# Performance work log

Measured on AMD Instinct MI355X. Metric: run time of the kernel, lower is better.

The kernel has to match this reference:

```python
import jax, jax.numpy as jnp
import numpy as np

B, T, IN, H, OUT = 64, 32, 256, 512, 256
M, W, R = 256, 64, 4            # nr_cells, cell_size, read_heads
NN_IN = IN + R * W              # 512
NN_OUT = H + R * W              # 768
IFACE = R * W + 3 * W + 5 * R + 3  # 471
CLIP = 20.0
DELTA = 1e-6


def setup_inputs():
    key = jax.random.key(0)
    ks = jax.random.split(key, 10)
    s = 0.05
    bound = float(np.sqrt(6.0 / (B * H + 2 * H)))  # xavier_uniform on (2,B,H)
    return {
        'x': jax.random.normal(ks[0], (B, T, IN), jnp.float32),
        'h0': jax.random.uniform(ks[1], (2, B, H), jnp.float32, -bound, bound),
        'Wih0': jax.random.normal(ks[2], (4 * H, NN_IN), jnp.float32) * s,
        'Whh0': jax.random.normal(ks[3], (4 * H, H), jnp.float32) * s,
        'bih0': jnp.zeros((4 * H,), jnp.float32),
        'bhh0': jnp.zeros((4 * H,), jnp.float32),
        'Wih1': jax.random.normal(ks[4], (4 * H, H), jnp.float32) * s,
        'Whh1': jax.random.normal(ks[5], (4 * H, H), jnp.float32) * s,
        'bih1': jnp.zeros((4 * H,), jnp.float32),
        'bhh1': jnp.zeros((4 * H,), jnp.float32),
        'Wif': jax.random.normal(ks[6], (IFACE, H), jnp.float32) * s,
        'bif': jnp.zeros((IFACE,), jnp.float32),
        'Wout': jax.random.normal(ks[7], (OUT, NN_OUT), jnp.float32) * s,
        'bout': jnp.zeros((OUT,), jnp.float32),
    }


def _lstm_cell(x, h, c, Wih, Whh, bih, bhh):
    g = x @ Wih.T + bih + h @ Whh.T + bhh
    i, f, gg, o = jnp.split(g, 4, axis=1)  # torch gate order i,f,g,o
    c = jax.nn.sigmoid(f) * c + jax.nn.sigmoid(i) * jnp.tanh(gg)
    h = jax.nn.sigmoid(o) * jnp.tanh(c)
    return h, c


def _content_weights(mem, keys, strengths):
    # mem: (b,M,W), keys: (b,K,W), strengths: (b,K) -> softmax over M
    mem_n = mem / (jnp.linalg.norm(mem, axis=2, keepdims=True) + DELTA)
    key_n = keys / (jnp.linalg.norm(keys, axis=2, keepdims=True) + DELTA)
    sim = jnp.einsum('bkw,bmw->bkm', key_n, mem_n)
    return jax.nn.softmax(sim * strengths[..., None], axis=2)


def _memory_step(xi, mem, link, prec, rw, ww, usage):
    b = xi.shape[0]
    o = 0
    rk = jnp.tanh(xi[:, :R * W].reshape(b, R, W)); o = R * W
    rs = jax.nn.softplus(xi[:, o:o + R]); o += R
    wk = jnp.tanh(xi[:, o:o + W]).reshape(b, 1, W); o += W
    ws = jax.nn.softplus(xi[:, o])[:, None]; o += 1
    ev = jax.nn.sigmoid(xi[:, o:o + W]); o += W
    wv = jnp.tanh(xi[:, o:o + W]); o += W
    fg = jax.nn.sigmoid(xi[:, o:o + R]); o += R
    ag = jax.nn.sigmoid(xi[:, o])[:, None]; o += 1
    wg = jax.nn.sigmoid(xi[:, o])[:, None]; o += 1
    rm = jax.nn.softmax(xi[:, o:o + 3 * R].reshape(b, R, 3), axis=2)

    # usage update (uses OLD read/write weights); single write head
    usage = usage + (1.0 - usage) * ww
    psi = jnp.prod(1.0 - fg[:, :, None] * rw, axis=1)
    usage = usage * psi

    # write content addressing on OLD memory
    wcw = _content_weights(mem, wk, ws)[:, 0]  # (b,M)

    # allocation by ascending sort of usage (exclusive cumprod)
    u = DELTA + (1.0 - DELTA) * usage
    phi = jnp.argsort(u, axis=1)
    sorted_u = jnp.take_along_axis(u, phi, axis=1)
    excl = jnp.cumprod(jnp.concatenate([jnp.ones((b, 1), u.dtype), sorted_u], axis=1), axis=1)[:, :-1]
    sorted_alloc = (1.0 - sorted_u) * excl
    alloc = jnp.take_along_axis(sorted_alloc, jnp.argsort(phi, axis=1), axis=1)

    ww = wg * (ag * alloc + (1.0 - ag) * wcw)  # (b,M)

    # erase + write
    mem = mem * (1.0 - ww[:, :, None] * ev[:, None, :]) + ww[:, :, None] * wv[:, None, :]

    # temporal link matrix + precedence
    prev_scale = 1.0 - ww[:, :, None] - ww[:, None, :]
    link = prev_scale * link + ww[:, :, None] * prec[:, None, :]
    link = link * (1.0 - jnp.eye(M, dtype=link.dtype))
    prec = (1.0 - ww.sum(axis=1, keepdims=True)) * prec + ww

    # read: directional weights use NEW link and OLD read weights; content uses NEW memory
    rcw = _content_weights(mem, rk, rs)               # (b,R,M)
    fwd = jnp.einsum('bij,brj->bri', link, rw)
    bwd = jnp.einsum('brj,bji->bri', rw, link)
    rw = rm[:, :, 0:1] * bwd + rm[:, :, 1:2] * fwd + rm[:, :, 2:3] * rcw
    rvec = jnp.einsum('brm,bmw->brw', rw, mem).reshape(b, R * W)
    return rvec, mem, link, prec, rw, ww, usage


def reference(x, h0, Wih0, Whh0, bih0, bhh0, Wih1, Whh1, bih1, bhh1, Wif, bif, Wout, bout):
    b = x.shape[0]
    lr0 = jnp.zeros((b, R * W), x.dtype)  # initial last_read; NOTE: source concatenates this
    # initial zero last_read to EVERY timestep's controller input (inputs built upfront)
    carry0 = (h0[0], h0[0], h0[1], h0[1],
              jnp.full((b, M, W), DELTA, x.dtype),   # memory
              jnp.zeros((b, M, M), x.dtype),          # link matrix
              jnp.zeros((b, M), x.dtype),             # precedence
              jnp.full((b, R, M), DELTA, x.dtype),    # read weights
              jnp.full((b, M), DELTA, x.dtype),       # write weights
              jnp.zeros((b, M), x.dtype))             # usage

    def step(carry, x_t):
        h0_, c0_, h1_, c1_, mem, link, prec, rw, ww, usage = carry
        inp = jnp.concatenate([x_t, lr0], axis=1)
        h0_, c0_ = _lstm_cell(inp, h0_, c0_, Wih0, Whh0, bih0, bhh0)
        h1_, c1_ = _lstm_cell(h0_, h1_, c1_, Wih1, Whh1, bih1, bhh1)
        out = jnp.clip(h1_, -CLIP, CLIP)
        xi = out @ Wif.T + bif
        rvec, mem, link, prec, rw, ww, usage = _memory_step(xi, mem, link, prec, rw, ww, usage)
        o_t = jnp.concatenate([out, rvec], axis=1)  # (b, NN_OUT)
        return (h0_, c0_, h1_, c1_, mem, link, prec, rw, ww, usage), o_t

    _, ys = jax.lax.scan(step, carry0, jnp.swapaxes(x, 0, 1))  # (T,b,NN_OUT)
    outputs = jnp.tanh(ys) @ Wout.T + bout  # Dropout(p=0) -> Tanh -> Linear
    return jnp.swapaxes(outputs, 0, 1)      # (b,T,OUT)
```

## Files before the change

### kernel.cpp

```cpp
#include <hip/hip_runtime.h>
#include <hip/hip_bf16.h>
#include <math.h>


typedef __bf16 bf16_t;
typedef __attribute__((ext_vector_type(8))) __bf16 bf16x8;
typedef __attribute__((ext_vector_type(4))) float f32x4;

#define B_    64
#define T_    32
#define IN_   256
#define H_    512
#define M_    256
#define W_    64
#define R_    4
#define IFACE_ 471
#define DELTA_ 1e-6f

#define OFF_H0SEQ  (0L)
#define SZ_H0SEQ   (32L*64*512*2)
#define OFF_OUTSEQ (OFF_H0SEQ + SZ_H0SEQ)
#define SZ_OUTSEQ  (32L*64*512*2)
#define OFF_H0BUF  (OFF_OUTSEQ + SZ_OUTSEQ)
#define SZ_HBUF    (2L*64*512*2)
// ... 135 lines not shown
  v0=__expf(v0-mx); v1=__expf(v1-mx); v2=__expf(v2-mx); v3=__expf(v3-mx);
  float s = v0+v1+v2+v3;
  #pragma unroll
  for (int off=32; off; off>>=1) s += __shfl_xor(s, off, 64);
  float inv = frcp(s);
  a[lane]=v0*inv; a[64+lane]=v1*inv; a[128+lane]=v2*inv; a[192+lane]=v3*inv;
}

struct ProdShm {
  bf16_t wpool[66560];
  float  cst[64][16];
  float  bias[4][16];
};
struct ConsShm {
  float smem[256][65];
  float xib[480];
  float rkn4r[2][65][4];
  float wkn[64], ev_[64], wvv[64];
  float rs_[4], fg_[4], rm_[4][3];
  float wsS, agS, wgS, wwsumS;
  float invn[256], wcw[256];
  float usage[256], uu[256], su[256], scanA[256];
  int   rank_[256];
  float ww_[256], prec_[256];
  float rw_[4][256];
  float rw4[256][4];
  float fwd_[4][256], bwd_[4][256], rcw_[4][256];
  bf16_t rwb[4][264];
  bf16_t wwb[256], precb[256];
  float p2cT[2][264];
  float p5cT[5][2][264];
  float rvp[8][4][64];
};
union ShUnion { ProdShm p; ConsShm c; };

__global__ __launch_bounds__(512) void k_main(
    const bf16_t* __restrict__ xb, const bf16_t* __restrict__ h0b,
    const bf16_t* __restrict__ W0, const bf16_t* __restrict__ W1,
    const bf16_t* __restrict__ W2, const bf16_t* __restrict__ W3,
    const float* __restrict__ bs0, const float* __restrict__ bs1,
    const bf16_t* __restrict__ Wifp, const float* __restrict__ bifp,
    bf16_t* __restrict__ h0buf, bf16_t* __restrict__ h1buf,
    bf16_t* __restrict__ h0seq, bf16_t* __restrict__ outseq,
    float* __restrict__ XI, float* __restrict__ RVEC,
    unsigned* __restrict__ flg)
{
  __shared__ ShUnion sh;
  const int bid = blockIdx.x;
  const int tid = threadIdx.x, lane = tid & 63, wv = tid >> 6;
  const int m16 = lane & 15, q = lane >> 4;

  if (bid < 64){
    ProdShm& P = sh.p;
    const int layer = bid >> 5;
    const int u0 = (bid & 31) * 16;

    if (!layer){
      for (int i = tid; i < 64*32; i += 512){
        int rl = i >> 5, c8 = (i & 31)*8;
        int grow = (rl >> 4)*512 + u0 + (rl & 15);
        *(bf16x8*)&P.wpool[rl*264 + c8] = *(const bf16x8*)(W0 + (size_t)grow*512 + c8);
      }
      for (int i = tid; i < 64*64; i += 512){
        int rl = i >> 6, c8 = (i & 63)*8;
        int grow = (rl >> 4)*512 + u0 + (rl & 15);
        *(bf16x8*)&P.wpool[16896 + rl*520 + c8] = *(const bf16x8*)(W1 + (size_t)grow*512 + c8);
      }
    } else {
      for (int i = tid; i < 64*64; i += 512){
        int rl = i >> 6, c8 = (i & 63)*8;
        int grow = (rl >> 4)*512 + u0 + (rl & 15);
        *(bf16x8*)&P.wpool[rl*520 + c8]         = *(const bf16x8*)(W2 + (size_t)grow*512 + c8);
        *(bf16x8*)&P.wpool[33280 + rl*520 + c8] = *(const bf16x8*)(W3 + (size_t)grow*512 + c8);
      }
    }
    for (int i = tid; i < 64*16; i += 512){
      int b = i >> 4, n = i & 15;
      P.cst[b][n] = (float)h0b[layer*(64*512) + b*512 + u0 + n];
    }
    if (tid < 64){
      int G = tid >> 4, n = tid & 15;
      const float* bs = layer ? bs1 : bs0;
      P.bias[G][n] = bs[G*512 + u0 + n];
    }
    __syncthreads();

    bf16_t* hbuf = layer ? h1buf : h0buf;

    for (int ps = 0; ps <= 33; ++ps){
      if (wv < 4){
        const int t = layer ? (ps - 1) : ps;
        const bool active = layer ? (ps >= 1 && ps <= 32) : (ps < 32);
        if (active){
          const int p = t & 1;
          const bf16_t* hin = hbuf + p*(64*512);
          bf16_t* hout = hbuf + (p^1)*(64*512);
          const int b0 = wv * 16;

          f32x4 acc[4];
          #pragma unroll
          for (int G = 0; G < 4; ++G){ float bv = P.bias[G][m16]; acc[G] = (f32x4){bv,bv,bv,bv}; }

          if (!layer){
            #pragma unroll 2
            for (int kt = 0; kt < 8; ++kt){
              bf16x8 a = *(const bf16x8*)(xb + ((size_t)(b0+m16)*T_ + t)*IN_ + kt*32 + q*8);
              #pragma unroll
              for (int G = 0; G < 4; ++G)
                acc[G] = __builtin_amdgcn_mfma_f32_16x16x32_bf16(
                    a, *(const bf16x8*)&P.wpool[(G*16+m16)*264 + kt*32 + q*8], acc[G], 0, 0, 0);
            }
            #pragma unroll 4
            for (int kt = 0; kt < 16; ++kt){
              bf16x8 a = *(const bf16x8*)(hin + (b0+m16)*512 + kt*32 + q*8);
              #pragma unroll
              for (int G = 0; G < 4; ++G)
                acc[G] = __builtin_amdgcn_mfma_f32_16x16x32_bf16(
                    a, *(const bf16x8*)&P.wpool[16896 + (G*16+m16)*520 + kt*32 + q*8], acc[G], 0, 0, 0);
            }
          } else {
            #pragma unroll 4
            for (int kt = 0; kt < 16; ++kt){
              bf16x8 a = *(const bf16x8*)(h0seq + ((size_t)t*64 + b0+m16)*512 + kt*32 + q*8);
              #pragma unroll
              for (int G = 0; G < 4; ++G)
                acc[G] = __builtin_amdgcn_mfma_f32_16x16x32_bf16(
                    a, *(const bf16x8*)&P.wpool[(G*16+m16)*520 + kt*32 + q*8], acc[G], 0, 0, 0);
            }
            #pragma unroll 4
            for (int kt = 0; kt < 16; ++kt){
              bf16x8 a = *(const bf16x8*)(hin + (b0+m16)*512 + kt*32 + q*8);
              #pragma unroll
              for (int G = 0; G < 4; ++G)
                acc[G] = __builtin_amdgcn_mfma_f32_16x16x32_bf16(
                    a, *(const bf16x8*)&P.wpool[33280 + (G*16+m16)*520 + kt*32 + q*8], acc[G], 0, 0, 0);
            }
          }
          #pragma unroll
          for (int v = 0; v < 4; ++v){
            int b = b0 + q*4 + v;
            float gi = acc[0][v], gf = acc[1][v], gg = acc[2][v], go = acc[3][v];
            float c_ = sigf(gf)*P.cst[b][m16] + sigf(gi)*tanh_f(gg);
            P.cst[b][m16] = c_;
            float h = sigf(go)*tanh_f(c_);
            bf16_t hb = (bf16_t)h;
            hout[b*512 + u0 + m16] = hb;
            if (!layer) h0seq[((size_t)t*64 + b)*512 + u0 + m16] = hb;
            else        outseq[((size_t)t*64 + b)*512 + u0 + m16] = hb;
          }
        }
      } else if (ps >= 2 && bid < 30){
        const int t2 = ps - 2;
        const int b0 = (wv - 4) * 16;
        const int r = bid*16 + m16;
        float bv = bifp[r];
        f32x4 acc = {bv,bv,bv,bv};
        const bf16_t* arow = outseq + ((size_t)t2*64 + b0 + m16)*512 + q*8;
        const bf16_t* brow = Wifp + (size_t)r*512 + q*8;
        #pragma unroll 4
        for (int kt = 0; kt < 16; ++kt){
          acc = __builtin_amdgcn_mfma_f32_16x16x32_bf16(
              *(const bf16x8*)(arow + kt*32), *(const bf16x8*)(brow + kt*32), acc, 0, 0, 0);
        }
        #pragma unroll
        for (int v = 0; v < 4; ++v)
          XI[((size_t)t2*64 + b0 + q*4 + v)*480 + r] = acc[v];
      }
      flagbar(flg, bid, (unsigned)(ps + 1), tid, lane, wv);
    }
  } else {
    ConsShm& S = sh.c;
    const int b = bid - 64;
    const int quad = lane >> 4, li = lane & 15;

    bf16x8 rowL[2][8], colL[2][8];
    #pragma unroll
    for (int g = 0; g < 2; ++g)
      #pragma unroll
      for (int ch = 0; ch < 8; ++ch)
        #pragma unroll
        for (int z = 0; z < 8; ++z){ rowL[g][ch][z] = (bf16_t)0.0f; colL[g][ch][z] = (bf16_t)0.0f; }

    float mr[32];
    #pragma unroll
    for (int z = 0; z < 32; ++z) mr[z] = DELTA_;

    if (tid < 256){
      S.ww_[tid] = DELTA_; S.usage[tid] = 0.0f; S.prec_[tid] = 0.0f;
      S.invn[tid] = 1.0f/(fsqrt_(64.0f*DELTA_*DELTA_) + DELTA_);
      S.wwb[tid] = (bf16_t)DELTA_; S.precb[tid] = (bf16_t)0.0f;
      #pragma unroll
      for (int r = 0; r < 4; ++r) S.rw_[r][tid] = DELTA_;
    }
    for (int i = tid; i < 4*264; i += 512) ((bf16_t*)S.rwb)[i] = (bf16_t)DELTA_;
    for (int i = tid; i < 256*65; i += 512) ((float*)S.smem)[i] = DELTA_;
    __syncthreads();

    const int mH = tid >> 1, q2 = tid & 1;

    for (int t = 0; t < 32; ++t){
      { const unsigned tgt = (unsigned)(t + 3);
        if (wv == 0){
          for (;;){
            unsigned f = flag_ld(flg + (size_t)lane*16);
            if (__all(f >= tgt)) break;
            __builtin_amdgcn_s_sleep(2);
          }
          __builtin_amdgcn_fence(__ATOMIC_ACQUIRE, "agent");
        }
        __syncthreads();
      }
      if (tid < IFACE_) S.xib[tid] = XI[((size_t)t*64 + b)*480 + tid];
      __syncthreads();

      if (wv < 4){
        float v = tanh_f(S.xib[wv*64 + lane]);
        float s = wred(v*v);
        float vn = v * frcp(fsqrt_(s) + DELTA_);
        S.rkn4r[0][lane][wv] = vn; S.rkn4r[1][lane][wv] = vn;
      } else if (wv == 4){
        float v = tanh_f(S.xib[260 + lane]);
        float s = wred(v*v);
        S.wkn[lane] = v * frcp(fsqrt_(s) + DELTA_);
      } else if (wv == 5){ S.ev_[lane] = sigf(S.xib[325 + lane]);
      } else if (wv == 6){ S.wvv[lane] = tanh_f(S.xib[389 + lane]);
      } else {
        if (lane < 4)        S.rs_[lane] = softplusf(S.xib[256 + lane]);
        else if (lane == 4)  S.wsS = softplusf(S.xib[324]);
        else if (lane < 9)   S.fg_[lane-5] = sigf(S.xib[453 + (lane-5)]);
        else if (lane == 9)  S.agS = sigf(S.xib[457]);
        else if (lane == 10) S.wgS = sigf(S.xib[458]);
        else if (lane >= 16 && lane < 20){
          int r = lane - 16;
          float a0 = S.xib[459+r*3], a1 = S.xib[459+r*3+1], a2 = S.xib[459+r*3+2];
          float mx = fmaxf(a0, fmaxf(a1, a2));
          float e0 = __expf(a0-mx), e1 = __expf(a1-mx), e2 = __expf(a2-mx);
          float inv = frcp(e0+e1+e2);
          S.rm_[r][0]=e0*inv; S.rm_[r][1]=e1*inv; S.rm_[r][2]=e2*inv;
        }
      }
      __syncthreads();

      if (tid < 256){
        int m = tid;
        float us = S.usage[m] + (1.0f - S.usage[m])*S.ww_[m];
        float psi = (1.0f - S.fg_[0]*S.rw_[0][m]) * (1.0f - S.fg_[1]*S.rw_[1][m])
                  * (1.0f - S.fg_[2]*S.rw_[2][m]) * (1.0f - S.fg_[3]*S.rw_[3][m]);
        us *= psi;
        S.usage[m] = us;
        S.uu[m] = DELTA_ + (1.0f - DELTA_)*us;
      }
      { float acc = 0.0f;
        #pragma unroll
        for (int it = 0; it < 32; ++it){
          int w = q2*32 + it;
          acc += mr[it] * S.wkn[w];
        }
        S.p2cT[q2][mH] = acc; }
      __syncthreads();

      if (wv == 0){
        #pragma unroll
        for (int z = 0; z < 4; ++z){
          int m = z*64 + lane;
          S.wcw[m] = S.wsS * (S.p2cT[0][m] + S.p2cT[1][m]) * S.invn[m];
        }
        softmax256_wave(S.wcw, lane);
      } else if (tid >= 256){
        const int i = tid - 256;
        const float ui = S.uu[i];
        int cnt = 0;
        #pragma unroll 8
        for (int k = 0; k < 64; ++k){
          f32x4 u4 = *(const f32x4*)&S.uu[k*4];
          #pragma unroll
          for (int z = 0; z < 4; ++z){
            int j = k*4 + z; float uj = u4[z];
            cnt += (uj < ui || (uj == ui && j < i)) ? 1 : 0;
          }
        }
        S.rank_[i] = cnt;
        S.su[cnt] = ui;
      }
      __syncthreads();

      if (wv == 0){
        int base = lane*4;
        float v0 = S.su[base], v1 = S.su[base+1], v2 = S.su[base+2];
        float p1 = v0*v1, p2 = p1*v2, p3 = p2*S.su[base+3];
        float sc = p3;
        #pragma unroll
        for (int off = 1; off < 64; off <<= 1){
          float n = __shfl_up(sc, off, 64);
          if (lane >= off) sc *= n;
        }
        float exch = __shfl_up(sc, 1, 64);
        if (lane == 0) exch = 1.0f;
        S.scanA[base] = exch; S.scanA[base+1] = exch*v0;
        S.scanA[base+2] = exch*p1; S.scanA[base+3] = exch*p2;
      }
      __syncthreads();

      { const int m = mH;
        float al = (1.0f - S.uu[m]) * S.scanA[S.rank_[m]];
        float wm = S.wgS*(S.agS*al + (1.0f - S.agS)*S.wcw[m]);
        if (q2 == 0){ S.ww_[m] = wm; S.wwb[m] = (bf16_t)wm; }
        float s2 = 0.0f, sr0 = 0.0f, sr1 = 0.0f, sr2 = 0.0f, sr3 = 0.0f;
        #pragma unroll
        for (int it = 0; it < 32; ++it){
          int w = q2*32 + it;
          float mn = mr[it]*(1.0f - wm*S.ev_[w]) + wm*S.wvv[w];
          mr[it] = mn;
          S.smem[m][w] = mn;
          s2 += mn*mn;
          f32x4 rk = *(const f32x4*)&S.rkn4r[q2][w][0];
          sr0 += mn*rk[0]; sr1 += mn*rk[1]; sr2 += mn*rk[2]; sr3 += mn*rk[3];
        }
        S.p5cT[0][q2][m] = s2;
        S.p5cT[1][q2][m] = sr0; S.p5cT[2][q2][m] = sr1;
        S.p5cT[3][q2][m] = sr2; S.p5cT[4][q2][m] = sr3; }
      __syncthreads();

      if (tid < 256){
        int m = tid;
        float s2 = S.p5cT[0][0][m] + S.p5cT[0][1][m];
        float inv = frcp(fsqrt_(s2) + DELTA_);
        S.invn[m] = inv;
        #pragma unroll
        for (int r = 0; r < 4; ++r){
          float sr = S.p5cT[r+1][0][m] + S.p5cT[r+1][1][m];
          S.rcw_[r][m] = S.rs_[r]*sr*inv;
        }
      } else if (wv == 4){
        float s = wred(S.ww_[lane] + S.ww_[64+lane] + S.ww_[128+lane] + S.ww_[192+lane]);
        if (lane == 0) S.wwsumS = s;
      }
      __syncthreads();

      { float wown[2], pown[2], alpha[2];
        #pragma unroll
        for (int g = 0; g < 2; ++g){
          int o = wv*32 + g*16 + li;
          wown[g] = (float)S.wwb[o]; pown[g] = (float)S.precb[o];
          alpha[g] = 1.0f - wown[g];
        }
        f32x4 facc[2] = {{0,0,0,0},{0,0,0,0}}, bacc[2] = {{0,0,0,0},{0,0,0,0}};
        #pragma unroll
        for (int ch = 0; ch < 8; ++ch){
          const int cbase = ch*32 + quad*8;
          bf16x8 rwf = *(const bf16x8*)&S.rwb[li & 3][cbase];
          bf16x8 wwv = *(const bf16x8*)&S.wwb[cbase];
          bf16x8 pcv = *(const bf16x8*)&S.precb[cbase];
          float wcf[8], pcf[8];
          #pragma unroll
          for (int jj = 0; jj < 8; ++jj){ wcf[jj] = (float)wwv[jj]; pcf[jj] = (float)pcv[jj]; }
          #pragma unroll
          for (int g = 0; g < 2; ++g){
            const int o = wv*32 + g*16 + li;
            bf16x8 rl = rowL[g][ch];
            bf16x8 cl = colL[g][ch];
            #pragma unroll
            for (int jj = 0; jj < 8; ++jj){
              const int c = cbase + jj;
              float s = alpha[g] - wcf[jj];
              float vr = s*(float)rl[jj] + wown[g]*pcf[jj];
              float vc = s*(float)cl[jj] + wcf[jj]*pown[g];
              if (c == o){ vr = 0.0f; vc = 0.0f; }
              rl[jj] = (bf16_t)vr;
              cl[jj] = (bf16_t)vc;
            }
            rowL[g][ch] = rl; colL[g][ch] = cl;
            facc[g] = __builtin_amdgcn_mfma_f32_16x16x32_bf16(rl, rwf, facc[g], 0, 0, 0);
            bacc[g] = __builtin_amdgcn_mfma_f32_16x16x32_bf16(rwf, cl, bacc[g], 0, 0, 0);
          }
        }
        #pragma unroll
        for (int g = 0; g < 2; ++g){
          if (li < 4){
            #pragma unroll
            for (int z = 0; z < 4; ++z) S.fwd_[li][wv*32 + g*16 + quad*4 + z] = facc[g][z];
          }
          if (quad == 0){
            #pragma unroll
            for (int z = 0; z < 4; ++z) S.bwd_[z][wv*32 + g*16 + li] = bacc[g][z];
          }
        }
      }
      __syncthreads();

      if (wv < 4) softmax256_wave(S.rcw_[wv], lane);
      else {
        int m = tid - 256;
        float p = (1.0f - S.wwsumS)*S.prec_[m] + S.ww_[m];
        S.prec_[m] = p;
        S.precb[m] = (bf16_t)p;
      }
      __syncthreads();

      { int r = tid >> 7, m0 = (tid & 127)*2;
        #pragma unroll
        for (int z = 0; z < 2; ++z){
          int m = m0 + z;
          float v = S.rm_[r][0]*S.bwd_[r][m] + S.rm_[r][1]*S.fwd_[r][m] + S.rm_[r][2]*S.rcw_[r][m];
          S.rw_[r][m] = v;
          S.rw4[m][r] = v;
          S.rwb[r][m] = (bf16_t)v;
        } }
      __syncthreads();

      { float r0 = 0, r1 = 0, r2 = 0, r3 = 0;
        #pragma unroll
        for (int k = 0; k < 32; ++k){
          int m = wv*32 + k;
          f32x4 r4 = *(const f32x4*)&S.rw4[m][0];
          float mv = S.smem[m][lane];
          r0 += r4[0]*mv; r1 += r4[1]*mv; r2 += r4[2]*mv; r3 += r4[3]*mv;
        }
        S.rvp[wv][0][lane] = r0; S.rvp[wv][1][lane] = r1;
        S.rvp[wv][2][lane] = r2; S.rvp[wv][3][lane] = r3; }
      __syncthreads();

      if (tid < 256){
        const int w = tid & 63, r = tid >> 6;
        float v = 0.0f;
        #pragma unroll
        for (int c = 0; c < 8; ++c) v += S.rvp[c][r][w];
        RVEC[((size_t)t*64 + b)*256 + tid] = v;
      }
      __syncthreads();
    }
  }
}

__global__ void k_tanhy(const bf16_t* __restrict__ outseq, const float* __restrict__ RVEC,
                        bf16_t* __restrict__ Y){
  const int n = 2048*768;
  for (int i = blockIdx.x*blockDim.x + threadIdx.x; i < n; i += gridDim.x*blockDim.x){
    int row = i / 768, j = i - row*768;
    float v = (j < 512) ? (float)outseq[(size_t)row*512 + j] : RVEC[(size_t)row*256 + (j - 512)];
    Y[i] = (bf16_t)tanh_f(v);
  }
}

__global__ __launch_bounds__(256,1) void k_out(
    const bf16_t* __restrict__ Y, const bf16_t* __restrict__ Woutb,
    const float* __restrict__ boutf, void* __restrict__ dout,
    const int* __restrict__ flag)
{
  const int mf = *flag;
  const int mt = blockIdx.x;
  const int tid = threadIdx.x, lane = tid & 63, wv = tid >> 6;
  const int nt = blockIdx.y*4 + wv;
  const int m16 = lane & 15, q = lane >> 4;
  const int o = nt*16 + m16;
  float bv = boutf[o];
  f32x4 acc = {bv,bv,bv,bv};
  const bf16_t* arow = Y + (size_t)(mt*16 + m16)*768 + q*8;
  const bf16_t* brow = Woutb + (size_t)o*768 + q*8;
  for (int kt = 0; kt < 24; ++kt){
    acc = __builtin_amdgcn_mfma_f32_16x16x32_bf16(
        *(const bf16x8*)(arow + kt*32), *(const bf16x8*)(brow + kt*32), acc, 0, 0, 0);
  }
  #pragma unroll
// ... 10 lines not shown
                              void* d_out, int out_size, void* d_ws, size_t ws_size,
                              hipStream_t stream)
{
  char* ws = (char*)d_ws;
  bf16_t* H0SEQ  = (bf16_t*)(ws + OFF_H0SEQ);
  bf16_t* OUTSEQ = (bf16_t*)(ws + OFF_OUTSEQ);
  bf16_t* H0BUF  = (bf16_t*)(ws + OFF_H0BUF);
  bf16_t* H1BUF  = (bf16_t*)(ws + OFF_H1BUF);
  float*  XI     = (float*) (ws + OFF_XI);
  float*  RVEC   = (float*) (ws + OFF_RVEC);
  bf16_t* YBF    = (bf16_t*)(ws + OFF_YBF);
  unsigned* BAR  = (unsigned*)(ws + OFF_BAR);
  int*    FLAG   = (int*)   (ws + OFF_BAR + 8);
  bf16_t* XB     = (bf16_t*)(ws + OFF_XB);
  bf16_t* H0B    = (bf16_t*)(ws + OFF_H0B);
  bf16_t* W0     = (bf16_t*)(ws + OFF_W0);
  bf16_t* W1     = (bf16_t*)(ws + OFF_W1);
  bf16_t* W2     = (bf16_t*)(ws + OFF_W2);
  bf16_t* W3     = (bf16_t*)(ws + OFF_W3);
  bf16_t* WIFP   = (bf16_t*)(ws + OFF_WIF);
  bf16_t* WOUTB  = (bf16_t*)(ws + OFF_WOUTB);
  float*  BS0    = (float*) (ws + OFF_BS0);
  float*  BS1    = (float*) (ws + OFF_BS1);
  float*  BIFP   = (float*) (ws + OFF_BIF);
  float*  BOUTF  = (float*) (ws + OFF_BOUTF);
  unsigned* FLG  = (unsigned*)(ws + OFF_FLG);

  k_detect<<<1, 256, 0, stream>>>((const unsigned short*)d_in[0], FLAG, BAR, FLG);
  k_convert<<<dim3(256, 9), 256, 0, stream>>>(
      d_in[0], d_in[1], d_in[2], d_in[3], d_in[4], d_in[5], d_in[6],
      d_in[7], d_in[8], d_in[9], d_in[10], d_in[11], d_in[12], d_in[13],
      XB, H0B, H0BUF, H1BUF, W0, W1, W2, W3, WIFP, WOUTB,
      BS0, BS1, BIFP, BOUTF, FLAG);
  k_main<<<128, 512, 0, stream>>>(XB, H0B, W0, W1, W2, W3, BS0, BS1,
                                  WIFP, BIFP, H0BUF, H1BUF, H0SEQ, OUTSEQ,
                                  XI, RVEC, FLG);
  k_tanhy<<<512, 256, 0, stream>>>(OUTSEQ, RVEC, YBF);
  k_out<<<dim3(128, 4), 256, 0, stream>>>(YBF, WOUTB, BOUTF, d_out, FLAG);
}
```

Measured before the change: 1.057 ms.

## Split fused persistent LSTM/memory kernel into separate LSTM, interface and memory kernels

Replaces the single persistent kernel, where 64 producer blocks ran the two LSTM layers and 64 consumer blocks ran the DNC memory update behind flag-based polling, with three sequential launches. The LSTM kernel keeps the grid-wide flag barrier but drops the interface-projection waves. The interface GEMM becomes its own fully parallel grid over timesteps. The memory kernel runs all 32 steps without waiting on flags. This removes cross-block polling and the idle half-warps in producer blocks, but gives up the overlap between the LSTM recurrence and the memory recurrence, so the two serial chains now run back to back.

```diff
diff --git a/kernel.cpp b/kernel.cpp
--- a/kernel.cpp
+++ b/kernel.cpp
@@ -191,403 +191,396 @@
   float p5cT[5][2][264];
   float rvp[8][4][64];
 };
-union ShUnion { ProdShm p; ConsShm c; };
-
-__global__ __launch_bounds__(512) void k_main(
+
+__global__ __launch_bounds__(256) void k_lstm(
     const bf16_t* __restrict__ xb, const bf16_t* __restrict__ h0b,
     const bf16_t* __restrict__ W0, const bf16_t* __restrict__ W1,
     const bf16_t* __restrict__ W2, const bf16_t* __restrict__ W3,
     const float* __restrict__ bs0, const float* __restrict__ bs1,
-    const bf16_t* __restrict__ Wifp, const float* __restrict__ bifp,
     bf16_t* __restrict__ h0buf, bf16_t* __restrict__ h1buf,
     bf16_t* __restrict__ h0seq, bf16_t* __restrict__ outseq,
-    float* __restrict__ XI, float* __restrict__ RVEC,
     unsigned* __restrict__ flg)
 {
-  __shared__ ShUnion sh;
+  __shared__ ProdShm P;
   const int bid = blockIdx.x;
   const int tid = threadIdx.x, lane = tid & 63, wv = tid >> 6;
   const int m16 = lane & 15, q = lane >> 4;
-
-  if (bid < 64){
-    ProdShm& P = sh.p;
-    const int layer = bid >> 5;
-    const int u0 = (bid & 31) * 16;
-
-    if (!layer){
-      for (int i = tid; i < 64*32; i += 512){
-        int rl = i >> 5, c8 = (i & 31)*8;
-        int grow = (rl >> 4)*512 + u0 + (rl & 15);
-        *(bf16x8*)&P.wpool[rl*264 + c8] = *(const bf16x8*)(W0 + (size_t)grow*512 + c8);
-      }
-      for (int i = tid; i < 64*64; i += 512){
-        int rl = i >> 6, c8 = (i & 63)*8;
-        int grow = (rl >> 4)*512 + u0 + (rl & 15);
-        *(bf16x8*)&P.wpool[16896 + rl*520 + c8] = *(const bf16x8*)(W1 + (size_t)grow*512 + c8);
-      }
-    } else {
-      for (int i = tid; i < 64*64; i += 512){
-        int rl = i >> 6, c8 = (i & 63)*8;
-        int grow = (rl >> 4)*512 + u0 + (rl & 15);
-        *(bf16x8*)&P.wpool[rl*520 + c8]         = *(const bf16x8*)(W2 + (size_t)grow*512 + c8);
-        *(bf16x8*)&P.wpool[33280 + rl*520 + c8] = *(const bf16x8*)(W3 + (size_t)grow*512 + c8);
-      }
-    }
-    for (int i = tid; i < 64*16; i += 512){
-      int b = i >> 4, n = i & 15;
-      P.cst[b][n] = (float)h0b[layer*(64*512) + b*512 + u0 + n];
-    }
-    if (tid < 64){
-      int G = tid >> 4, n = tid & 15;
-      const float* bs = layer ? bs1 : bs0;
-      P.bias[G][n] = bs[G*512 + u0 + n];
-    }
-    __syncthreads();
-
-    bf16_t* hbuf = layer ? h1buf : h0buf;
-
-    for (int ps = 0; ps <= 33; ++ps){
-      if (wv < 4){
-        const int t = layer ? (ps - 1) : ps;
-        const bool active = layer ? (ps >= 1 && ps <= 32) : (ps < 32);
-        if (active){
-          const int p = t & 1;
-          const bf16_t* hin = hbuf + p*(64*512);
-          bf16_t* hout = hbuf + (p^1)*(64*512);
-          const int b0 = wv * 16;
-
-          f32x4 acc[4];
+  const int layer = bid >> 5;
+  const int u0 = (bid & 31) * 16;
+
+  if (!layer){
+    for (int i = tid; i < 64*32; i += 256){
+      int rl = i >> 5, c8 = (i & 31)*8;
+      int grow = (rl >> 4)*512 + u0 + (rl & 15);
+      *(bf16x8*)&P.wpool[rl*264 + c8] = *(const bf16x8*)(W0 + (size_t)grow*512 + c8);
+    }
+    for (int i = tid; i < 64*64; i += 256){
+      int rl = i >> 6, c8 = (i & 63)*8;
+      int grow = (rl >> 4)*512 + u0 + (rl & 15);
+      *(bf16x8*)&P.wpool[16896 + rl*520 + c8] = *(const bf16x8*)(W1 + (size_t)grow*512 + c8);
+    }
+  } else {
+    for (int i = tid; i < 64*64; i += 256){
+      int rl = i >> 6, c8 = (i & 63)*8;
+      int grow = (rl >> 4)*512 + u0 + (rl & 15);
+      *(bf16x8*)&P.wpool[rl*520 + c8]         = *(const bf16x8*)(W2 + (size_t)grow*512 + c8);
+      *(bf16x8*)&P.wpool[33280 + rl*520 + c8] = *(const bf16x8*)(W3 + (size_t)grow*512 + c8);
+    }
+  }
+  for (int i = tid; i < 64*16; i += 256){
+    int b = i >> 4, n = i & 15;
+    P.cst[b][n] = (float)h0b[layer*(64*512) + b*512 + u0 + n];
+  }
+  if (tid < 64){
+    int G = tid >> 4, n = tid & 15;
+    const float* bs = layer ? bs1 : bs0;
+    P.bias[G][n] = bs[G*512 + u0 + n];
+  }
+  __syncthreads();
+
+  bf16_t* hbuf = layer ? h1buf : h0buf;
+
+  for (int ps = 0; ps <= 32; ++ps){
+    const int t = layer ? (ps - 1) : ps;
+    const bool active = layer ? (ps >= 1) : (ps < 32);
+    if (active){
+      const int p = t & 1;
+      const bf16_t* hin = hbuf + p*(64*512);
+      bf16_t* hout = hbuf + (p^1)*(64*512);
+      const int b0 = wv * 16;
+
+      f32x4 acc[4];
+      #pragma unroll
+      for (int G = 0; G < 4; ++G){ float bv = P.bias[G][m16]; acc[G] = (f32x4){bv,bv,bv,bv}; }
+
+      if (!layer){
+        #pragma unroll 2
+        for (int kt = 0; kt < 8; ++kt){
+          bf16x8 a = *(const bf16x8*)(xb + ((size_t)(b0+m16)*T_ + t)*IN_ + kt*32 + q*8);
           #pragma unroll
-          for (int G = 0; G < 4; ++G){ float bv = P.bias[G][m16]; acc[G] = (f32x4){bv,bv,bv,bv}; }
-
-          if (!layer){
-            #pragma unroll 2
-            for (int kt = 0; kt < 8; ++kt){
-              bf16x8 a = *(const bf16x8*)(xb + ((size_t)(b0+m16)*T_ + t)*IN_ + kt*32 + q*8);
-              #pragma unroll
-              for (int G = 0; G < 4; ++G)
-                acc[G] = __builtin_amdgcn_mfma_f32_16x16x32_bf16(
-                    a, *(const bf16x8*)&P.wpool[(G*16+m16)*264 + kt*32 + q*8], acc[G], 0, 0, 0);
-            }
-            #pragma unroll 4
-            for (int kt = 0; kt < 16; ++kt){
-              bf16x8 a = *(const bf16x8*)(hin + (b0+m16)*512 + kt*32 + q*8);
-              #pragma unroll
-              for (int G = 0; G < 4; ++G)
-                acc[G] = __builtin_amdgcn_mfma_f32_16x16x32_bf16(
-                    a, *(const bf16x8*)&P.wpool[16896 + (G*16+m16)*520 + kt*32 + q*8], acc[G], 0, 0, 0);
-            }
-          } else {
-            #pragma unroll 4
-            for (int kt = 0; kt < 16; ++kt){
-              bf16x8 a = *(const bf16x8*)(h0seq + ((size_t)t*64 + b0+m16)*512 + kt*32 + q*8);
-              #pragma unroll
-              for (int G = 0; G < 4; ++G)
-                acc[G] = __builtin_amdgcn_mfma_f32_16x16x32_bf16(
-                    a, *(const bf16x8*)&P.wpool[(G*16+m16)*520 + kt*32 + q*8], acc[G], 0, 0, 0);
-            }
-            #pragma unroll 4
-            for (int kt = 0; kt < 16; ++kt){
-              bf16x8 a = *(const bf16x8*)(hin + (b0+m16)*512 + kt*32 + q*8);
-              #pragma unroll
-              for (int G = 0; G < 4; ++G)
-                acc[G] = __builtin_amdgcn_mfma_f32_16x16x32_bf16(
-                    a, *(const bf16x8*)&P.wpool[33280 + (G*16+m16)*520 + kt*32 + q*8], acc[G], 0, 0, 0);
-            }
-          }
-          #pragma unroll
-          for (int v = 0; v < 4; ++v){
-            int b = b0 + q*4 + v;
-            float gi = acc[0][v], gf = acc[1][v], gg = acc[2][v], go = acc[3][v];
-            float c_ = sigf(gf)*P.cst[b][m16] + sigf(gi)*tanh_f(gg);
-            P.cst[b][m16] = c_;
-            float h = sigf(go)*tanh_f(c_);
-            bf16_t hb = (bf16_t)h;
-            hout[b*512 + u0 + m16] = hb;
-            if (!layer) h0seq[((size_t)t*64 + b)*512 + u0 + m16] = hb;
-            else        outseq[((size_t)t*64 + b)*512 + u0 + m16] = hb;
-          }
-        }
-      } else if (ps >= 2 && bid < 30){
-        const int t2 = ps - 2;
-        const int b0 = (wv - 4) * 16;
-        const int r = bid*16 + m16;
-        float bv = bifp[r];
-        f32x4 acc = {bv,bv,bv,bv};
-        const bf16_t* arow = outseq + ((size_t)t2*64 + b0 + m16)*512 + q*8;
-        const bf16_t* brow = Wifp + (size_t)r*512 + q*8;
+          for (int G = 0; G < 4; ++G)
+            acc[G] = __builtin_amdgcn_mfma_f32_16x16x32_bf16(
+                a, *(const bf16x8*)&P.wpool[(G*16+m16)*264 + kt*32 + q*8], acc[G], 0, 0, 0);
+        }
         #pragma unroll 4
         for (int kt = 0; kt < 16; ++kt){
-          acc = __builtin_amdgcn_mfma_f32_16x16x32_bf16(
-              *(const bf16x8*)(arow + kt*32), *(const bf16x8*)(brow + kt*32), acc, 0, 0, 0);
-        }
-        #pragma unroll
-        for (int v = 0; v < 4; ++v)
-          XI[((size_t)t2*64 + b0 + q*4 + v)*480 + r] = acc[v];
-      }
-      flagbar(flg, bid, (unsigned)(ps + 1), tid, lane, wv);
-    }
-  } else {
-    ConsShm& S = sh.c;
-    const int b = bid - 64;
-    const int quad = lane >> 4, li = lane & 15;
-
-    bf16x8 rowL[2][8], colL[2][8];
+          bf16x8 a = *(const bf16x8*)(hin + (b0+m16)*512 + kt*32 + q*8);
+          #pragma unroll
+          for (int G = 0; G < 4; ++G)
+            acc[G] = __builtin_amdgcn_mfma_f32_16x16x32_bf16(
+                a, *(const bf16x8*)&P.wpool[16896 + (G*16+m16)*520 + kt*32 + q*8], acc[G], 0, 0, 0);
+        }
+      } else {
+        #pragma unroll 4
+        for (int kt = 0; kt < 16; ++kt){
+          bf16x8 a = *(const bf16x8*)(h0seq + ((size_t)t*64 + b0+m16)*512 + kt*32 + q*8);
+          #pragma unroll
+          for (int G = 0; G < 4; ++G)
+            acc[G] = __builtin_amdgcn_mfma_f32_16x16x32_bf16(
+                a, *(const bf16x8*)&P.wpool[(G*16+m16)*520 + kt*32 + q*8], acc[G], 0, 0, 0);
+        }
+        #pragma unroll 4
+        for (int kt = 0; kt < 16; ++kt){
+          bf16x8 a = *(const bf16x8*)(hin + (b0+m16)*512 + kt*32 + q*8);
+          #pragma unroll
+          for (int G = 0; G < 4; ++G)
+            acc[G] = __builtin_amdgcn_mfma_f32_16x16x32_bf16(
+                a, *(const bf16x8*)&P.wpool[33280 + (G*16+m16)*520 + kt*32 + q*8], acc[G], 0, 0, 0);
+        }
+      }
+      #pragma unroll
+      for (int v = 0; v < 4; ++v){
+        int b = b0 + q*4 + v;
+        float gi = acc[0][v], gf = acc[1][v], gg = acc[2][v], go = acc[3][v];
+        float c_ = sigf(gf)*P.cst[b][m16] + sigf(gi)*tanh_f(gg);
+        P.cst[b][m16] = c_;
+        float h = sigf(go)*tanh_f(c_);
+        bf16_t hb = (bf16_t)h;
+        hout[b*512 + u0 + m16] = hb;
+        if (!layer) h0seq[((size_t)t*64 + b)*512 + u0 + m16] = hb;
+        else        outseq[((size_t)t*64 + b)*512 + u0 + m16] = hb;
+      }
+    }
+    if (ps < 32) flagbar(flg, bid, (unsigned)(ps + 1), tid, lane, wv);
+  }
+}
+
+__global__ __launch_bounds__(256) void k_xi(
+    const bf16_t* __restrict__ outseq, const bf16_t* __restrict__ Wifp,
+    const float* __restrict__ bifp, float* __restrict__ XI)
+{
+  const int rt = blockIdx.x;
+  const int t2 = blockIdx.y;
+  const int tid = threadIdx.x, lane = tid & 63, wv = tid >> 6;
+  const int m16 = lane & 15, q = lane >> 4;
+  const int b0 = wv * 16;
+  const int r = rt*16 + m16;
+  float bv = bifp[r];
+  f32x4 acc = {bv,bv,bv,bv};
+  const bf16_t* arow = outseq + ((size_t)t2*64 + b0 + m16)*512 + q*8;
+  const bf16_t* brow = Wifp + (size_t)r*512 + q*8;
+  #pragma unroll 4
+  for (int kt = 0; kt < 16; ++kt){
+    acc = __builtin_amdgcn_mfma_f32_16x16x32_bf16(
+        *(const bf16x8*)(arow + kt*32), *(const bf16x8*)(brow + kt*32), acc, 0, 0, 0);
+  }
+  #pragma unroll
+  for (int v = 0; v < 4; ++v)
+    XI[((size_t)t2*64 + b0 + q*4 + v)*480 + r] = acc[v];
+}
+
+__global__ __launch_bounds__(512) void k_mem(
+    const float* __restrict__ XI, float* __restrict__ RVEC)
+{
+  __shared__ ConsShm S;
+  const int b = blockIdx.x;
+  const int tid = threadIdx.x, lane = tid & 63, wv = tid >> 6;
+  const int quad = lane >> 4, li = lane & 15;
+
+  bf16x8 rowL[2][8], colL[2][8];
+  #pragma unroll
+  for (int g = 0; g < 2; ++g)
     #pragma unroll
-    for (int g = 0; g < 2; ++g)
-      #pragma unroll
-      for (int ch = 0; ch < 8; ++ch)
-        #pragma unroll
-        for (int z = 0; z < 8; ++z){ rowL[g][ch][z] = (bf16_t)0.0f; colL[g][ch][z] = (bf16_t)0.0f; }
-
-    float mr[32];
+    for (int ch = 0; ch < 8; ++ch)
+      #pragma unroll
+      for (int z = 0; z < 8; ++z){ rowL[g][ch][z] = (bf16_t)0.0f; colL[g][ch][z] = (bf16_t)0.0f; }
+
+  float mr[32];
+  #pragma unroll
+  for (int z = 0; z < 32; ++z) mr[z] = DELTA_;
+
+  if (tid < 256){
+    S.ww_[tid] = DELTA_; S.usage[tid] = 0.0f; S.prec_[tid] = 0.0f;
+    S.invn[tid] = 1.0f/(fsqrt_(64.0f*DELTA_*DELTA_) + DELTA_);
+    S.wwb[tid] = (bf16_t)DELTA_; S.precb[tid] = (bf16_t)0.0f;
     #pragma unroll
-    for (int z = 0; z < 32; ++z) mr[z] = DELTA_;
+    for (int r = 0; r < 4; ++r) S.rw_[r][tid] = DELTA_;
+  }
+  for (int i = tid; i < 4*264; i += 512) ((bf16_t*)S.rwb)[i] = (bf16_t)DELTA_;
+  for (int i = tid; i < 256*65; i += 512) ((float*)S.smem)[i] = DELTA_;
+  __syncthreads();
+
+  const int mH = tid >> 1, q2 = tid & 1;
+
+  for (int t = 0; t < 32; ++t){
+    if (tid < IFACE_) S.xib[tid] = XI[((size_t)t*64 + b)*480 + tid];
+    __syncthreads();
+
+    if (wv < 4){
+      float v = tanh_f(S.xib[wv*64 + lane]);
+      float s = wred(v*v);
+      float vn = v * frcp(fsqrt_(s) + DELTA_);
+      S.rkn4r[0][lane][wv] = vn; S.rkn4r[1][lane][wv] = vn;
+    } else if (wv == 4){
+      float v = tanh_f(S.xib[260 + lane]);
+      float s = wred(v*v);
+      S.wkn[lane] = v * frcp(fsqrt_(s) + DELTA_);
+    } else if (wv == 5){ S.ev_[lane] = sigf(S.xib[325 + lane]);
+    } else if (wv == 6){ S.wvv[lane] = tanh_f(S.xib[389 + lane]);
+    } else {
+      if (lane < 4)        S.rs_[lane] = softplusf(S.xib[256 + lane]);
+      else if (lane == 4)  S.wsS = softplusf(S.xib[324]);
+      else if (lane < 9)   S.fg_[lane-5] = sigf(S.xib[453 + (lane-5)]);
+      else if (lane == 9)  S.agS = sigf(S.xib[457]);
+      else if (lane == 10) S.wgS = sigf(S.xib[458]);
+      else if (lane >= 16 && lane < 20){
+        int r = lane - 16;
+        float a0 = S.xib[459+r*3], a1 = S.xib[459+r*3+1], a2 = S.xib[459+r*3+2];
+        float mx = fmaxf(a0, fmaxf(a1, a2));
+        float e0 = __expf(a0-mx), e1 = __expf(a1-mx), e2 = __expf(a2-mx);
+        float inv = frcp(e0+e1+e2);
+        S.rm_[r][0]=e0*inv; S.rm_[r][1]=e1*inv; S.rm_[r][2]=e2*inv;
+      }
+    }
+    __syncthreads();
 
     if (tid < 256){
-      S.ww_[tid] = DELTA_; S.usage[tid] = 0.0f; S.prec_[tid] = 0.0f;
-      S.invn[tid] = 1.0f/(fsqrt_(64.0f*DELTA_*DELTA_) + DELTA_);
-      S.wwb[tid] = (bf16_t)DELTA_; S.precb[tid] = (bf16_t)0.0f;
-      #pragma unroll
-      for (int r = 0; r < 4; ++r) S.rw_[r][tid] = DELTA_;
-    }
-    for (int i = tid; i < 4*264; i += 512) ((bf16_t*)S.rwb)[i] = (bf16_t)DELTA_;
-    for (int i = tid; i < 256*65; i += 512) ((float*)S.smem)[i] = DELTA_;
-    __syncthreads();
-
-    const int mH = tid >> 1, q2 = tid & 1;
-
-    for (int t = 0; t < 32; ++t){
-      { const unsigned tgt = (unsigned)(t + 3);
-        if (wv == 0){
-          for (;;){
-            unsigned f = flag_ld(flg + (size_t)lane*16);
-            if (__all(f >= tgt)) break;
-            __builtin_amdgcn_s_sleep(2);
-          }
-          __builtin_amdgcn_fence(__ATOMIC_ACQUIRE, "agent");
-        }
-        __syncthreads();
-      }
-      if (tid < IFACE_) S.xib[tid] = XI[((size_t)t*64 + b)*480 + tid];
-      __syncthreads();
-
-      if (wv < 4){
-        float v = tanh_f(S.xib[wv*64 + lane]);
-        float s = wred(v*v);
-        float vn = v * frcp(fsqrt_(s) + DELTA_);
-        S.rkn4r[0][lane][wv] = vn; S.rkn4r[1][lane][wv] = vn;
-      } else if (wv == 4){
-        float v = tanh_f(S.xib[260 + lane]);
-        float s = wred(v*v);
-        S.wkn[lane] = v * frcp(fsqrt_(s) + DELTA_);
-      } else if (wv == 5){ S.ev_[lane] = sigf(S.xib[325 + lane]);
-      } else if (wv == 6){ S.wvv[lane] = tanh_f(S.xib[389 + lane]);
-      } else {
-        if (lane < 4)        S.rs_[lane] = softplusf(S.xib[256 + lane]);
-        else if (lane == 4)  S.wsS = softplusf(S.xib[324]);
-        else if (lane < 9)   S.fg_[lane-5] = sigf(S.xib[453 + (lane-5)]);
-        else if (lane == 9)  S.agS = sigf(S.xib[457]);
-        else if (lane == 10) S.wgS = sigf(S.xib[458]);
-        else if (lane >= 16 && lane < 20){
-          int r = lane - 16;
-          float a0 = S.xib[459+r*3], a1 = S.xib[459+r*3+1], a2 = S.xib[459+r*3+2];
-          float mx = fmaxf(a0, fmaxf(a1, a2));
-          float e0 = __expf(a0-mx), e1 = __expf(a1-mx), e2 = __expf(a2-mx);
-          float inv = frcp(e0+e1+e2);
-          S.rm_[r][0]=e0*inv; S.rm_[r][1]=e1*inv; S.rm_[r][2]=e2*inv;
-        }
-      }
-      __syncthreads();
-
-      if (tid < 256){
-        int m = tid;
-        float us = S.usage[m] + (1.0f - S.usage[m])*S.ww_[m];
-        float psi = (1.0f - S.fg_[0]*S.rw_[0][m]) * (1.0f - S.fg_[1]*S.rw_[1][m])
-                  * (1.0f - S.fg_[2]*S.rw_[2][m]) * (1.0f - S.fg_[3]*S.rw_[3][m]);
-        us *= psi;
-        S.usage[m] = us;
-        S.uu[m] = DELTA_ + (1.0f - DELTA_)*us;
-      }
-      { float acc = 0.0f;
-        #pragma unroll
-        for (int it = 0; it < 32; ++it){
-          int w = q2*32 + it;
-          acc += mr[it] * S.wkn[w];
-        }
-        S.p2cT[q2][mH] = acc; }
-      __syncthreads();
-
-      if (wv == 0){
+      int m = tid;
+      float us = S.usage[m] + (1.0f - S.usage[m])*S.ww_[m];
+      float psi = (1.0f - S.fg_[0]*S.rw_[0][m]) * (1.0f - S.fg_[1]*S.rw_[1][m])
+                * (1.0f - S.fg_[2]*S.rw_[2][m]) * (1.0f - S.fg_[3]*S.rw_[3][m]);
+      us *= psi;
+      S.usage[m] = us;
+      S.uu[m] = DELTA_ + (1.0f - DELTA_)*us;
+    }
+    { float acc = 0.0f;
+      #pragma unroll
+      for (int it = 0; it < 32; ++it){
+        int w = q2*32 + it;
+        acc += mr[it] * S.wkn[w];
+      }
+      S.p2cT[q2][mH] = acc; }
+    __syncthreads();
+
+    if (wv == 0){
+      #pragma unroll
+      for (int z = 0; z < 4; ++z){
+        int m = z*64 + lane;
+        S.wcw[m] = S.wsS * (S.p2cT[0][m] + S.p2cT[1][m]) * S.invn[m];
+      }
+      softmax256_wave(S.wcw, lane);
+    } else if (tid >= 256){
+      const int i = tid - 256;
+      const float ui = S.uu[i];
+      int cnt = 0;
+      #pragma unroll 8
+      for (int k = 0; k < 64; ++k){
+        f32x4 u4 = *(const f32x4*)&S.uu[k*4];
         #pragma unroll
         for (int z = 0; z < 4; ++z){
-          int m = z*64 + lane;
-          S.wcw[m] = S.wsS * (S.p2cT[0][m] + S.p2cT[1][m]) * S.invn[m];
-        }
-        softmax256_wave(S.wcw, lane);
-      } else if (tid >= 256){
-        const int i = tid - 256;
-        const float ui = S.uu[i];
-        int cnt = 0;
-        #pragma unroll 8
-        for (int k = 0; k < 64; ++k){
-          f32x4 u4 = *(const f32x4*)&S.uu[k*4];
-          #pragma unroll
-          for (int z = 0; z < 4; ++z){
-            int j = k*4 + z; float uj = u4[z];
-            cnt += (uj < ui || (uj == ui && j < i)) ? 1 : 0;
-          }
-        }
-        S.rank_[i] = cnt;
-        S.su[cnt] = ui;
-      }
-      __syncthreads();
-
-      if (wv == 0){
-        int base = lane*4;
-        float v0 = S.su[base], v1 = S.su[base+1], v2 = S.su[base+2];
-        float p1 = v0*v1, p2 = p1*v2, p3 = p2*S.su[base+3];
-        float sc = p3;
+          int j = k*4 + z; float uj = u4[z];
+          cnt += (uj < ui || (uj == ui && j < i)) ? 1 : 0;
+        }
+      }
+      S.rank_[i] = cnt;
+      S.su[cnt] = ui;
+    }
+    __syncthreads();
+
+    if (wv == 0){
+      int base = lane*4;
+      float v0 = S.su[base], v1 = S.su[base+1], v2 = S.su[base+2];
+      float p1 = v0*v1, p2 = p1*v2, p3 = p2*S.su[base+3];
+      float sc = p3;
+      #pragma unroll
+      for (int off = 1; off < 64; off <<= 1){
+        float n = __shfl_up(sc, off, 64);
+        if (lane >= off) sc *= n;
+      }
+      float exch = __shfl_up(sc, 1, 64);
+      if (lane == 0) exch = 1.0f;
+      S.scanA[base] = exch; S.scanA[base+1] = exch*v0;
+      S.scanA[base+2] = exch*p1; S.scanA[base+3] = exch*p2;
+    }
+    __syncthreads();
+
+    { const int m = mH;
+      float al = (1.0f - S.uu[m]) * S.scanA[S.rank_[m]];
+      float wm = S.wgS*(S.agS*al + (1.0f - S.agS)*S.wcw[m]);
+      if (q2 == 0){ S.ww_[m] = wm; S.wwb[m] = (bf16_t)wm; }
+      float s2 = 0.0f, sr0 = 0.0f, sr1 = 0.0f, sr2 = 0.0f, sr3 = 0.0f;
+      #pragma unroll
+      for (int it = 0; it < 32; ++it){
+        int w = q2*32 + it;
+        float mn = mr[it]*(1.0f - wm*S.ev_[w]) + wm*S.wvv[w];
+        mr[it] = mn;
+        S.smem[m][w] = mn;
+        s2 += mn*mn;
+        f32x4 rk = *(const f32x4*)&S.rkn4r[q2][w][0];
+        sr0 += mn*rk[0]; sr1 += mn*rk[1]; sr2 += mn*rk[2]; sr3 += mn*rk[3];
+      }
+      S.p5cT[0][q2][m] = s2;
+      S.p5cT[1][q2][m] = sr0; S.p5cT[2][q2][m] = sr1;
+      S.p5cT[3][q2][m] = sr2; S.p5cT[4][q2][m] = sr3; }
+    __syncthreads();
+
+    if (tid < 256){
+      int m = tid;
+      float s2 = S.p5cT[0][0][m] + S.p5cT[0][1][m];
+      float inv = frcp(fsqrt_(s2) + DELTA_);
+      S.invn[m] = inv;
+      #pragma unroll
+      for (int r = 0; r < 4; ++r){
+        float sr = S.p5cT[r+1][0][m] + S.p5cT[r+1][1][m];
+        S.rcw_[r][m] = S.rs_[r]*sr*inv;
+      }
+    } else if (wv == 4){
+      float s = wred(S.ww_[lane] + S.ww_[64+lane] + S.ww_[128+lane] + S.ww_[192+lane]);
+      if (lane == 0) S.wwsumS = s;
+    }
+    __syncthreads();
+
+    { float wown[2], pown[2], alpha[2];
+      #pragma unroll
+      for (int g = 0; g < 2; ++g){
+        int o = wv*32 + g*16 + li;
+        wown[g] = (float)S.wwb[o]; pown[g] = (float)S.precb[o];
+        alpha[g] = 1.0f - wown[g];
+      }
+      f32x4 facc[2] = {{0,0,0,0},{0,0,0,0}}, bacc[2] = {{0,0,0,0},{0,0,0,0}};
+      #pragma unroll
+      for (int ch = 0; ch < 8; ++ch){
+        const int cbase = ch*32 + quad*8;
+        bf16x8 rwf = *(const bf16x8*)&S.rwb[li & 3][cbase];
+        bf16x8 wwv = *(const bf16x8*)&S.wwb[cbase];
+        bf16x8 pcv = *(const bf16x8*)&S.precb[cbase];
+        float wcf[8], pcf[8];
         #pragma unroll
-        for (int off = 1; off < 64; off <<= 1){
-          float n = __shfl_up(sc, off, 64);
-          if (lane >= off) sc *= n;
-        }
-        float exch = __shfl_up(sc, 1, 64);
-        if (lane == 0) exch = 1.0f;
-        S.scanA[base] = exch; S.scanA[base+1] = exch*v0;
-        S.scanA[base+2] = exch*p1; S.scanA[base+3] = exch*p2;
-      }
-      __syncthreads();
-
-      { const int m = mH;
-        float al = (1.0f - S.uu[m]) * S.scanA[S.rank_[m]];
-        float wm = S.wgS*(S.agS*al + (1.0f - S.agS)*S.wcw[m]);
-        if (q2 == 0){ S.ww_[m] = wm; S.wwb[m] = (bf16_t)wm; }
-        float s2 = 0.0f, sr0 = 0.0f, sr1 = 0.0f, sr2 = 0.0f, sr3 = 0.0f;
-        #pragma unroll
-        for (int it = 0; it < 32; ++it){
-          int w = q2*32 + it;
-          float mn = mr[it]*(1.0f - wm*S.ev_[w]) + wm*S.wvv[w];
-          mr[it] = mn;
-          S.smem[m][w] = mn;
-          s2 += mn*mn;
-          f32x4 rk = *(const f32x4*)&S.rkn4r[q2][w][0];
-          sr0 += mn*rk[0]; sr1 += mn*rk[1]; sr2 += mn*rk[2]; sr3 += mn*rk[3];
-        }
-        S.p5cT[0][q2][m] = s2;
-        S.p5cT[1][q2][m] = sr0; S.p5cT[2][q2][m] = sr1;
-        S.p5cT[3][q2][m] = sr2; S.p5cT[4][q2][m] = sr3; }
-      __syncthreads();
-
-      if (tid < 256){
-        int m = tid;
-        float s2 = S.p5cT[0][0][m] + S.p5cT[0][1][m];
-        float inv = frcp(fsqrt_(s2) + DELTA_);
-        S.invn[m] = inv;
-        #pragma unroll
-        for (int r = 0; r < 4; ++r){
-          float sr = S.p5cT[r+1][0][m] + S.p5cT[r+1][1][m];
-          S.rcw_[r][m] = S.rs_[r]*sr*inv;
-        }
-      } else if (wv == 4){
-        float s = wred(S.ww_[lane] + S.ww_[64+lane] + S.ww_[128+lane] + S.ww_[192+lane]);
-        if (lane == 0) S.wwsumS = s;
-      }
-      __syncthreads();
-
-      { float wown[2], pown[2], alpha[2];
+        for (int jj = 0; jj < 8; ++jj){ wcf[jj] = (float)wwv[jj]; pcf[jj] = (float)pcv[jj]; }
         #pragma unroll
         for (int g = 0; g < 2; ++g){
-          int o = wv*32 + g*16 + li;
-          wown[g] = (float)S.wwb[o]; pown[g] = (float)S.precb[o];
-          alpha[g] = 1.0f - wown[g];
-        }
-        f32x4 facc[2] = {{0,0,0,0},{0,0,0,0}}, bacc[2] = {{0,0,0,0},{0,0,0,0}};
-        #pragma unroll
-        for (int ch = 0; ch < 8; ++ch){
-          const int cbase = ch*32 + quad*8;
-          bf16x8 rwf = *(const bf16x8*)&S.rwb[li & 3][cbase];
-          bf16x8 wwv = *(const bf16x8*)&S.wwb[cbase];
-          bf16x8 pcv = *(const bf16x8*)&S.precb[cbase];
-          float wcf[8], pcf[8];
+          const int o = wv*32 + g*16 + li;
+          bf16x8 rl = rowL[g][ch];
+          bf16x8 cl = colL[g][ch];
           #pragma unroll
-          for (int jj = 0; jj < 8; ++jj){ wcf[jj] = (float)wwv[jj]; pcf[jj] = (float)pcv[jj]; }
+          for (int jj = 0; jj < 8; ++jj){
+            const int c = cbase + jj;
+            float s = alpha[g] - wcf[jj];
+            float vr = s*(float)rl[jj] + wown[g]*pcf[jj];
+            float vc = s*(float)cl[jj] + wcf[jj]*pown[g];
+            if (c == o){ vr = 0.0f; vc = 0.0f; }
+            rl[jj] = (bf16_t)vr;
+            cl[jj] = (bf16_t)vc;
+          }
+          rowL[g][ch] = rl; colL[g][ch] = cl;
+          facc[g] = __builtin_amdgcn_mfma_f32_16x16x32_bf16(rl, rwf, facc[g], 0, 0, 0);
+          bacc[g] = __builtin_amdgcn_mfma_f32_16x16x32_bf16(rwf, cl, bacc[g], 0, 0, 0);
+        }
+      }
+      #pragma unroll
+      for (int g = 0; g < 2; ++g){
+        if (li < 4){
           #pragma unroll
-          for (int g = 0; g < 2; ++g){
-            const int o = wv*32 + g*16 + li;
-            bf16x8 rl = rowL[g][ch];
-            bf16x8 cl = colL[g][ch];
-            #pragma unroll
-            for (int jj = 0; jj < 8; ++jj){
-              const int c = cbase + jj;
-              float s = alpha[g] - wcf[jj];
-              float vr = s*(float)rl[jj] + wown[g]*pcf[jj];
-              float vc = s*(float)cl[jj] + wcf[jj]*pown[g];
-              if (c == o){ vr = 0.0f; vc = 0.0f; }
-              rl[jj] = (bf16_t)vr;
-              cl[jj] = (bf16_t)vc;
-            }
-            rowL[g][ch] = rl; colL[g][ch] = cl;
-            facc[g] = __builtin_amdgcn_mfma_f32_16x16x32_bf16(rl, rwf, facc[g], 0, 0, 0);
-            bacc[g] = __builtin_amdgcn_mfma_f32_16x16x32_bf16(rwf, cl, bacc[g], 0, 0, 0);
-          }
-        }
-        #pragma unroll
-        for (int g = 0; g < 2; ++g){
-          if (li < 4){
-            #pragma unroll
-            for (int z = 0; z < 4; ++z) S.fwd_[li][wv*32 + g*16 + quad*4 + z] = facc[g][z];
-          }
-          if (quad == 0){
-            #pragma unroll
-            for (int z = 0; z < 4; ++z) S.bwd_[z][wv*32 + g*16 + li] = bacc[g][z];
-          }
-        }
-      }
-      __syncthreads();
-
-      if (wv < 4) softmax256_wave(S.rcw_[wv], lane);
-      else {
-        int m = tid - 256;
-        float p = (1.0f - S.wwsumS)*S.prec_[m] + S.ww_[m];
-        S.prec_[m] = p;
-        S.precb[m] = (bf16_t)p;
-      }
-      __syncthreads();
-
-      { int r = tid >> 7, m0 = (tid & 127)*2;
-        #pragma unroll
-        for (int z = 0; z < 2; ++z){
-          int m = m0 + z;
-          float v = S.rm_[r][0]*S.bwd_[r][m] + S.rm_[r][1]*S.fwd_[r][m] + S.rm_[r][2]*S.rcw_[r][m];
-          S.rw_[r][m] = v;
-          S.rw4[m][r] = v;
-          S.rwb[r][m] = (bf16_t)v;
-        } }
-      __syncthreads();
-
-      { float r0 = 0, r1 = 0, r2 = 0, r3 = 0;
-        #pragma unroll
-        for (int k = 0; k < 32; ++k){
-          int m = wv*32 + k;
-          f32x4 r4 = *(const f32x4*)&S.rw4[m][0];
-          float mv = S.smem[m][lane];
-          r0 += r4[0]*mv; r1 += r4[1]*mv; r2 += r4[2]*mv; r3 += r4[3]*mv;
-        }
-        S.rvp[wv][0][lane] = r0; S.rvp[wv][1][lane] = r1;
-        S.rvp[wv][2][lane] = r2; S.rvp[wv][3][lane] = r3; }
-      __syncthreads();
-
-      if (tid < 256){
-        const int w = tid & 63, r = tid >> 6;
-        float v = 0.0f;
-        #pragma unroll
-        for (int c = 0; c < 8; ++c) v += S.rvp[c][r][w];
-        RVEC[((size_t)t*64 + b)*256 + tid] = v;
-      }
-      __syncthreads();
-    }
+          for (int z = 0; z < 4; ++z) S.fwd_[li][wv*32 + g*16 + quad*4 + z] = facc[g][z];
+        }
+        if (quad == 0){
+          #pragma unroll
+          for (int z = 0; z < 4; ++z) S.bwd_[z][wv*32 + g*16 + li] = bacc[g][z];
+        }
+      }
+    }
+    __syncthreads();
+
+    if (wv < 4) softmax256_wave(S.rcw_[wv], lane);
+    else {
+      int m = tid - 256;
+      float p = (1.0f - S.wwsumS)*S.prec_[m] + S.ww_[m];
+      S.prec_[m] = p;
+      S.precb[m] = (bf16_t)p;
+    }
+    __syncthreads();
+
+    { int r = tid >> 7, m0 = (tid & 127)*2;
+      #pragma unroll
+      for (int z = 0; z < 2; ++z){
+        int m = m0 + z;
+        float v = S.rm_[r][0]*S.bwd_[r][m] + S.rm_[r][1]*S.fwd_[r][m] + S.rm_[r][2]*S.rcw_[r][m];
+        S.rw_[r][m] = v;
+        S.rw4[m][r] = v;
+        S.rwb[r][m] = (bf16_t)v;
+      } }
+    __syncthreads();
+
+    { float r0 = 0, r1 = 0, r2 = 0, r3 = 0;
+      #pragma unroll
+      for (int k = 0; k < 32; ++k){
+        int m = wv*32 + k;
+        f32x4 r4 = *(const f32x4*)&S.rw4[m][0];
+        float mv = S.smem[m][lane];
+        r0 += r4[0]*mv; r1 += r4[1]*mv; r2 += r4[2]*mv; r3 += r4[3]*mv;
+      }
+      S.rvp[wv][0][lane] = r0; S.rvp[wv][1][lane] = r1;
+      S.rvp[wv][2][lane] = r2; S.rvp[wv][3][lane] = r3; }
+    __syncthreads();
+
+    if (tid < 256){
+      const int w = tid & 63, r = tid >> 6;
+      float v = 0.0f;
+      #pragma unroll
+      for (int c = 0; c < 8; ++c) v += S.rvp[c][r][w];
+      RVEC[((size_t)t*64 + b)*256 + tid] = v;
+    }
+    __syncthreads();
   }
 }
 
@@ -664,9 +657,10 @@
       d_in[7], d_in[8], d_in[9], d_in[10], d_in[11], d_in[12], d_in[13],
       XB, H0B, H0BUF, H1BUF, W0, W1, W2, W3, WIFP, WOUTB,
       BS0, BS1, BIFP, BOUTF, FLAG);
-  k_main<<<128, 512, 0, stream>>>(XB, H0B, W0, W1, W2, W3, BS0, BS1,
-                                  WIFP, BIFP, H0BUF, H1BUF, H0SEQ, OUTSEQ,
-                                  XI, RVEC, FLG);
+  k_lstm<<<64, 256, 0, stream>>>(XB, H0B, W0, W1, W2, W3, BS0, BS1,
+                                 H0BUF, H1BUF, H0SEQ, OUTSEQ, FLG);
+  k_xi<<<dim3(30, 32), 256, 0, stream>>>(OUTSEQ, WIFP, BIFP, XI);
+  k_mem<<<64, 512, 0, stream>>>(XI, RVEC);
   k_tanhy<<<512, 256, 0, stream>>>(OUTSEQ, RVEC, YBF);
   k_out<<<dim3(128, 4), 256, 0, stream>>>(YBF, WOUTB, BOUTF, d_out, FLAG);
 }
```

Result: slower. 1.344 ms (+27.1%).
